# Performance work log

Measured on AMD Instinct MI355X. Metric: run time of the kernel, lower is better.

The kernel has to match this reference:

```python
import jax, jax.numpy as jnp
import numpy as np

P = 16        # patch size
B = 32        # batch
HW = 224      # image height/width
EMB = 768     # embedding dim
CN = (512, 2048, 8192)  # cluster counts
D = 3 * P * P  # patch feature dim = 768


def setup_inputs() -> dict:
    key = jax.random.key(0)
    ks = jax.random.split(key, 7)
    return {
        "data": jax.random.normal(ks[0], (B, 3, HW, HW), jnp.float32),
        "c0": jax.random.normal(ks[1], (CN[0], D), jnp.float32),
        "c1": jax.random.normal(ks[2], (CN[1], D), jnp.float32),
        "c2": jax.random.normal(ks[3], (CN[2], D), jnp.float32),
        "e0": jax.random.normal(ks[4], (CN[0], EMB), jnp.float32),
        "e1": jax.random.normal(ks[5], (CN[1], EMB), jnp.float32),
        "e2": jax.random.normal(ks[6], (CN[2], EMB), jnp.float32),
    }


def _classify(x, center):
    scores = -2.0 * (x @ center.T) + jnp.sum(center * center, axis=-1)  # [b, n, K]
    cls = jnp.argmin(scores, axis=-1)                                   # [b, n]
    img = center[cls]                                                   # nearest-center gather
    return cls, x - img, img


def reference(data, c0, c1, c2, e0, e1, e2):
    b, c, h, w = data.shape
    hp = h // P
    wp = w // P
    # b c (h hp) (w wp) -> b (h w) (c hp wp)
    x = data.reshape(b, c, hp, P, wp, P).transpose(0, 2, 4, 1, 3, 5).reshape(b, hp * wp, c * P * P)

    cls0, diff, img0 = _classify(x, c0)
    cls1, diff, img1 = _classify(diff, c1)
    cls2, diff, img2 = _classify(diff, c2)

    # reconstruct image from summed center patches: b (h w) (c hp wp) -> b c (h hp) (w wp)
    img_sum = (img0 + img1 + img2).reshape(b, hp, wp, c, P, P).transpose(0, 3, 1, 4, 2, 5).reshape(b, c, h, w)
    # residual: b (h w) c -> b c h w
    diff_out = diff.reshape(b, hp, wp, -1).transpose(0, 3, 1, 2)

    # embedding lookups (the only grad-carrying path in the torch module)
    embed = e0[cls0] + e1[cls1] + e2[cls2]          # [b, hp*wp, EMB]
    embed = embed.reshape(b, hp, wp, -1).transpose(0, 3, 1, 2)  # [b, EMB, hp, wp]

    # quantization branch is under torch.no_grad()
    return (embed, jax.lax.stop_gradient(img_sum), jax.lax.stop_gradient(diff_out))
```

## Files before the change

kernel.cpp:

```cpp
#include <hip/hip_runtime.h>
#include <stdint.h>

#define BATCH 32
#define HWD 224
#define HP 14
#define NP (BATCH * HP * HP)
#define DIM 768
#define K0 512
#define K1 2048
#define K2 8192
#define KTOT (K0 + K1 + K2)

typedef unsigned long long ull;
typedef unsigned int uint;
typedef __attribute__((ext_vector_type(8))) short bf16x8;
typedef __attribute__((ext_vector_type(4))) float f32x4;

__device__ __forceinline__ uint fkey(float f) {
    uint u = __float_as_uint(f);
    return (u & 0x80000000u) ? ~u : (u | 0x80000000u);
}
__device__ __forceinline__ short f2bf(float f) {
    uint u = __float_as_uint(f);
    uint r = (u + 0x7fffu + ((u >> 16) & 1u)) >> 16;
    return (short)r;
}
__device__ __forceinline__ float bf2f(short h) {
    return __uint_as_float(((uint)(unsigned short)h) << 16);
}
__device__ __forceinline__ ull umin64(ull a, ull b) { return a < b ? a : b; }
__device__ __forceinline__ ull umax64(ull a, ull b) { return a > b ? a : b; }

__global__ void patchify_split_kernel(const float* __restrict__ data,
                                      short* __restrict__ xh, short* __restrict__ xl) {
    int gid = blockIdx.x * 256 + threadIdx.x;
    int d = gid % DIM;
    int p = gid / DIM;
    int b = p / 196; int t = p % 196; int i = t / 14, j = t % 14;
    int ch = d >> 8; int r = d & 255; int py = r >> 4; int px = r & 15;
    float v = data[((b * 3 + ch) * HWD + i * 16 + py) * HWD + j * 16 + px];
    short h = f2bf(v);
    xh[gid] = h;
    xl[gid] = f2bf(v - bf2f(h));
}

__global__ void cprep_all_kernel(const float* __restrict__ c0, const float* __restrict__ c1,
                                 const float* __restrict__ c2,
                                 short* __restrict__ ch, float* __restrict__ nrm) {
    int lane = threadIdx.x & 63;
    int row = blockIdx.x * 4 + (threadIdx.x >> 6);
    const float* src;
    if (row < K0)           src = c0 + (size_t)row * DIM;
    else if (row < K0 + K1) src = c1 + (size_t)(row - K0) * DIM;
    else                    src = c2 + (size_t)(row - K0 - K1) * DIM;
    float s = 0.f;
    #pragma unroll
    for (int i = 0; i < 12; ++i) {
        int d = lane + i * 64;
        float v = src[d];
        ch[(size_t)row * DIM + d] = f2bf(v);
        s += v * v;
    }
    #pragma unroll
    for (int off = 32; off; off >>= 1) s += __shfl_xor(s, off, 64);
    if (lane == 0) nrm[row] = s;
}

__global__ __launch_bounds__(256, 2) void classify16(
    const short* __restrict__ xh,
    const short* __restrict__ chv,
    const float* __restrict__ nrm,
    ull* __restrict__ partB, ull* __restrict__ partS2)
{
    constexpr int NHT = 8;
    constexpr int NB = 256;
    constexpr int CH0 = 512;
    constexpr int SLOTS = 512 + 128 * NHT;
    constexpr int NJ = 6;
    constexpr int GX = NP / 128;
    __shared__ __align__(16) short lds[3 * SLOTS * 8];

    int bx = blockIdx.x, by = blockIdx.y;
    if ((gridDim.y & 7) == 0) {
        int P = blockIdx.x + GX * blockIdx.y;
        int xcd = P & 7;
        int wofs = P >> 3;
        int ypx = gridDim.y >> 3;
        by = xcd * ypx + (wofs % ypx);
        bx = wofs / ypx;
    }

    const int tid = threadIdx.x;
    const int lane = tid & 63;
    const int w = tid >> 6;
    const int wm = w & 1, wn = w >> 1;
    const int pbase = bx * 128;
    const int n0 = by * NB;

    const short* gp[NJ];
    int ls[NJ];
    #pragma unroll
    for (int j = 0; j < NJ; ++j) {
        int g = j * 4 + w;
        const short* base; int rb, sb, t;
        if (g < 8) { base = xh;  rb = pbase; sb = 0;    t = g; }
        else       { base = chv; rb = n0;    sb = CH0;  t = g - 8; }
        gp[j] = base + (size_t)(rb + t * 16 + (lane & 15)) * DIM + ((lane >> 4) * 8);
        ls[j] = sb + t * 64;
    }

    f32x4 acc[4][NHT];
    #pragma unroll
    for (int i = 0; i < 4; ++i)
        #pragma unroll
        for (int u = 0; u < NHT; ++u) acc[i][u] = (f32x4){0.f, 0.f, 0.f, 0.f};

    auto stage = [&](int buf, int kt) {
        const int off = buf * SLOTS;
        #pragma unroll
        for (int j = 0; j < NJ; ++j) {
            __builtin_amdgcn_global_load_lds(
                (const __attribute__((address_space(1))) void*)(gp[j] + kt * 32),
                (__attribute__((address_space(3))) void*)(lds + (size_t)(off + ls[j]) * 8),
                16, 0, 0);
        }
    };
    auto compute = [&](int buf) {
        const bf16x8* Lc = (const bf16x8*)lds + buf * SLOTS;
        bf16x8 fxh[4];
        #pragma unroll
        for (int i = 0; i < 4; ++i)
            fxh[i] = Lc[(wm * 4 + i) * 64 + lane];
        #pragma unroll
        for (int u = 0; u < NHT; ++u) {
            bf16x8 fch = Lc[CH0 + (wn * NHT + u) * 64 + lane];
            #pragma unroll
            for (int i = 0; i < 4; ++i)
                acc[i][u] = __builtin_amdgcn_mfma_f32_16x16x32_bf16(fxh[i], fch, acc[i][u], 0, 0, 0);
        }
    };

    stage(0, 0);
    stage(1, 1);
    asm volatile("s_waitcnt vmcnt(6)" ::: "memory");
    __builtin_amdgcn_s_barrier();
    __builtin_amdgcn_sched_barrier(0);

    #pragma unroll 3
    for (int t = 0; t < 24; ++t) {
        if (t + 2 < 24) stage((t + 2) % 3, t + 2);
        compute(t % 3);
        if (t < 23) {
            if (t + 2 < 24) asm volatile("s_waitcnt vmcnt(6)" ::: "memory");
            else            asm volatile("s_waitcnt vmcnt(0)" ::: "memory");
            __builtin_amdgcn_s_barrier();
            __builtin_amdgcn_sched_barrier(0);
        }
    }

    float nor[NHT]; uint ncol[NHT];
    #pragma unroll
    for (int u = 0; u < NHT; ++u) {
        ncol[u] = (uint)(n0 + (wn * NHT + u) * 16 + (lane & 15));
        nor[u] = nrm[ncol[u]];
    }
    const int pw = 2 * gridDim.y;
    #pragma unroll
    for (int i = 0; i < 4; ++i) {
        #pragma unroll
        for (int reg = 0; reg < 4; ++reg) {
            ull b = ~0ull, s2 = ~0ull;
            #pragma unroll
            for (int u = 0; u < NHT; ++u) {
                float s = fmaf(-2.f, acc[i][u][reg], nor[u]);
                ull pk = ((ull)fkey(s) << 32) | ncol[u];
                ull nb = umin64(b, pk);
                s2 = umin64(s2, umax64(b, pk));
                b = nb;
            }
            #pragma unroll
            for (int off = 1; off <= 8; off <<= 1) {
                ull ob = __shfl_xor(b, off, 64);
                ull os2 = __shfl_xor(s2, off, 64);
                ull nb = umin64(b, ob);
                s2 = umin64(umin64(s2, os2), umax64(b, ob));
                b = nb;
            }
            if ((lane & 15) == 0) {
                int row = pbase + (wm * 4 + i) * 16 + (lane >> 4) * 4 + reg;
                size_t o = (size_t)row * pw + (size_t)by * 2 + wn;
                partB[o] = b;
                partS2[o] = s2;
            }
        }
    }
}

__global__ void merge_rescue_update(
    short* __restrict__ xh, short* __restrict__ xl,
    const float* __restrict__ cent, const float* __restrict__ nrm,
    const ull* __restrict__ partB, const ull* __restrict__ partS2,
    int nsplit, int* __restrict__ cls)
{
    int lane = threadIdx.x & 63;
    int p = blockIdx.x * 4 + (threadIdx.x >> 6);
    ull a = ~0ull, c = ~0ull;
    for (int j = lane; j < nsplit; j += 64) {
        ull b2 = partB[(size_t)p * nsplit + j];
        ull s2b = partS2[(size_t)p * nsplit + j];
        ull na = umin64(a, b2);
        c = umin64(umin64(c, s2b), umax64(a, b2));
        a = na;
    }
    int idx[4];
    #pragma unroll
    for (int r = 0; r < 4; ++r) {
        ull m = a;
        #pragma unroll
        for (int off = 32; off; off >>= 1) m = umin64(m, __shfl_xor(m, off, 64));
        idx[r] = (int)(m & 0xFFFFFFFFull);
        if (a == m) { a = c; c = ~0ull; }
    }
    float xv[12];
    #pragma unroll
    for (int i = 0; i < 12; ++i) {
        int d = lane + i * 64;
        xv[i] = bf2f(xh[(size_t)p * DIM + d]) + bf2f(xl[(size_t)p * DIM + d]);
    }
    float dot[4] = {0.f, 0.f, 0.f, 0.f};
    #pragma unroll
    for (int r = 0; r < 4; ++r) {
        const float* cr = cent + (size_t)idx[r] * DIM;
        #pragma unroll
        for (int i = 0; i < 12; ++i) dot[r] = fmaf(xv[i], cr[lane + i * 64], dot[r]);
    }
    #pragma unroll
    for (int r = 0; r < 4; ++r)
        #pragma unroll
        for (int off = 32; off; off >>= 1) dot[r] += __shfl_xor(dot[r], off, 64);
    ull best = ~0ull;
    #pragma unroll
    for (int r = 0; r < 4; ++r) {
        float sc = fmaf(-2.f, dot[r], nrm[idx[r]]);
        best = umin64(best, ((ull)fkey(sc) << 32) | (uint)idx[r]);
    }
    int cw = (int)(best & 0xFFFFFFFFull);
    if (lane == 0) cls[p] = cw;
    const float* cwr = cent + (size_t)cw * DIM;
    #pragma unroll
    for (int i = 0; i < 12; ++i) {
        int d = lane + i * 64;
        float nx = xv[i] - cwr[d];
        short h = f2bf(nx);
        xh[(size_t)p * DIM + d] = h;
        xl[(size_t)p * DIM + d] = f2bf(nx - bf2f(h));
    }
}

__global__ void embdiff_kernel(const short* __restrict__ xh, const short* __restrict__ xl,
    const int* __restrict__ cls0, const int* __restrict__ cls1, const int* __restrict__ cls2,
    const float* __restrict__ e0, const float* __restrict__ e1, const float* __restrict__ e2,
    float* __restrict__ out)
{
    __shared__ float s[196][65];
    int b = blockIdx.x / 12;
    int dc = (blockIdx.x % 12) * 64;
    int tid = threadIdx.x;
    int dl = tid & 63;
    for (int it = 0; it < 49; ++it) {
        int pl = it * 4 + (tid >> 6);
        int p = b * 196 + pl;
        int d = dc + dl;
        s[pl][dl] = e0[(size_t)cls0[p] * DIM + d] + e1[(size_t)cls1[p] * DIM + d]
                  + e2[(size_t)cls2[p] * DIM + d];
    }
    __syncthreads();
    if (tid < 196) {
        for (int d = 0; d < 64; ++d)
            out[((size_t)b * DIM + dc + d) * 196 + tid] = s[tid][d];
    }
    __syncthreads();
    for (int it = 0; it < 49; ++it) {
        int pl = it * 4 + (tid >> 6);
        size_t o = (size_t)(b * 196 + pl) * DIM + dc + dl;
        s[pl][dl] = bf2f(xh[o]) + bf2f(xl[o]);
    }
    __syncthreads();
    if (tid < 196) {
        float* od = out + 2 * (size_t)NP * DIM;
        for (int d = 0; d < 64; ++d)
            od[((size_t)b * DIM + dc + d) * 196 + tid] = s[tid][d];
    }
}

__global__ void img_kernel(
    const int* __restrict__ cls0, const int* __restrict__ cls1, const int* __restrict__ cls2,
    const float* __restrict__ c0, const float* __restrict__ c1, const float* __restrict__ c2,
    float* __restrict__ out)
{
    __shared__ float s[14][256];
    int bi = blockIdx.x;
    int b = bi / 42; int rem = bi % 42; int ch = rem / 14; int i = rem % 14;
    int tid = threadIdx.x;
    for (int j = 0; j < 14; ++j) {
        int p = b * 196 + i * 14 + j;
        int d = ch * 256 + tid;
        s[j][tid] = c0[(size_t)cls0[p] * DIM + d] + c1[(size_t)cls1[p] * DIM + d]
                  + c2[(size_t)cls2[p] * DIM + d];
    }
    __syncthreads();
    float* oi = out + (size_t)NP * DIM;
    if (tid < 224) {
        int j = tid >> 4, px = tid & 15;
        for (int py = 0; py < 16; ++py)
            oi[(((size_t)b * 3 + ch) * HWD + i * 16 + py) * HWD + tid] = s[j][py * 16 + px];
    }
}

extern "C" void kernel_launch(void* const* d_in, const int* in_sizes, int n_in,
                              void* d_out, int out_size, void* d_ws, size_t ws_size,
                              hipStream_t stream) {
    const float* data = (const float*)d_in[0];
    const float* c0 = (const float*)d_in[1];
    const float* c1 = (const float*)d_in[2];
    const float* c2 = (const float*)d_in[3];
    const float* e0 = (const float*)d_in[4];
    const float* e1 = (const float*)d_in[5];
    const float* e2 = (const float*)d_in[6];
    float* out = (float*)d_out;

    char* w = (char*)d_ws;
    short* xh = (short*)w;    w += (size_t)NP * DIM * 2;
    short* xl = (short*)w;    w += (size_t)NP * DIM * 2;
    short* chB = (short*)w;   w += (size_t)KTOT * DIM * 2;
    float* nrm = (float*)w;   w += (size_t)KTOT * 4;
    ull* partB = (ull*)w;     w += (size_t)NP * 128 * 8;
    ull* partS2 = (ull*)w;    w += (size_t)NP * 128 * 8;
    int* cls0 = (int*)w;      w += (size_t)NP * 4;
    int* cls1 = (int*)w;      w += (size_t)NP * 4;
    int* cls2 = (int*)w;      w += (size_t)NP * 4;

    patchify_split_kernel<<<(NP * DIM) / 256, 256, 0, stream>>>(data, xh, xl);
    cprep_all_kernel<<<KTOT / 4, 256, 0, stream>>>(c0, c1, c2, chB, nrm);

    classify16<<<dim3(NP / 128, K0 / 256), 256, 0, stream>>>(
        xh, chB, nrm, partB, partS2);
    merge_rescue_update<<<NP / 4, 256, 0, stream>>>(xh, xl, c0, nrm, partB, partS2, 4, cls0);

    classify16<<<dim3(NP / 128, K1 / 256), 256, 0, stream>>>(
        xh, chB + (size_t)K0 * DIM, nrm + K0, partB, partS2);
    merge_rescue_update<<<NP / 4, 256, 0, stream>>>(xh, xl, c1, nrm + K0, partB, partS2, 16, cls1);

    classify16<<<dim3(NP / 128, K2 / 256), 256, 0, stream>>>(
        xh, chB + (size_t)(K0 + K1) * DIM, nrm + K0 + K1, partB, partS2);
    merge_rescue_update<<<NP / 4, 256, 0, stream>>>(xh, xl, c2, nrm + K0 + K1, partB, partS2, 64, cls2);

    embdiff_kernel<<<BATCH * 12, 256, 0, stream>>>(xh, xl, cls0, cls1, cls2, e0, e1, e2, out);
    img_kernel<<<BATCH * 3 * 14, 256, 0, stream>>>(cls0, cls1, cls2, c0, c1, c2, out);
}
```

Baseline: 433.6 us.

## Switch classify GEMM to double-buffered LDS with 3 blocks per SM

Cuts the LDS staging ring from three buffers to two and raises launch bounds from 2 to 3 blocks per CU, so more waves can hide latency. Global load base pointers are made wave-uniform through readfirstlane and a shared per-lane offset, to save VGPRs. The loop now issues one stage ahead with plain __syncthreads instead of fine-grained vmcnt waits. Each wave has less prefetch depth, and every barrier now waits for the whole load to finish, which can expose memory latency.

```diff
diff --git a/kernel.cpp b/kernel.cpp
--- a/kernel.cpp
+++ b/kernel.cpp
@@ -66,7 +66,7 @@
     if (lane == 0) nrm[row] = s;
 }
 
-__global__ __launch_bounds__(256, 2) void classify16(
+__global__ __launch_bounds__(256, 3) void classify16(
     const short* __restrict__ xh,
     const short* __restrict__ chv,
     const float* __restrict__ nrm,
@@ -78,7 +78,7 @@
     constexpr int SLOTS = 512 + 128 * NHT;
     constexpr int NJ = 6;
     constexpr int GX = NP / 128;
-    __shared__ __align__(16) short lds[3 * SLOTS * 8];
+    __shared__ __align__(16) short lds[2 * SLOTS * 8];
 
     int bx = blockIdx.x, by = blockIdx.y;
     if ((gridDim.y & 7) == 0) {
@@ -97,16 +97,20 @@
     const int pbase = bx * 128;
     const int n0 = by * NB;
 
-    const short* gp[NJ];
-    int ls[NJ];
+    const short* gbase[NJ];
+    int lsl[NJ];
+    const int laneoff = (lane & 15) * DIM + ((lane >> 4) * 8);
     #pragma unroll
     for (int j = 0; j < NJ; ++j) {
         int g = j * 4 + w;
         const short* base; int rb, sb, t;
         if (g < 8) { base = xh;  rb = pbase; sb = 0;    t = g; }
         else       { base = chv; rb = n0;    sb = CH0;  t = g - 8; }
-        gp[j] = base + (size_t)(rb + t * 16 + (lane & 15)) * DIM + ((lane >> 4) * 8);
-        ls[j] = sb + t * 64;
+        ull b64 = (ull)(base + (size_t)(rb + t * 16) * DIM);
+        uint lo = __builtin_amdgcn_readfirstlane((uint)b64);
+        uint hi = __builtin_amdgcn_readfirstlane((uint)(b64 >> 32));
+        gbase[j] = (const short*)(((ull)hi << 32) | lo);
+        lsl[j] = __builtin_amdgcn_readfirstlane(sb + t * 64);
     }
 
     f32x4 acc[4][NHT];
@@ -120,8 +124,8 @@
         #pragma unroll
         for (int j = 0; j < NJ; ++j) {
             __builtin_amdgcn_global_load_lds(
-                (const __attribute__((address_space(1))) void*)(gp[j] + kt * 32),
-                (__attribute__((address_space(3))) void*)(lds + (size_t)(off + ls[j]) * 8),
+                (const __attribute__((address_space(1))) void*)(gbase[j] + laneoff + kt * 32),
+                (__attribute__((address_space(3))) void*)(lds + (size_t)(off + lsl[j]) * 8),
                 16, 0, 0);
         }
     };
@@ -141,21 +145,12 @@
     };
 
     stage(0, 0);
-    stage(1, 1);
-    asm volatile("s_waitcnt vmcnt(6)" ::: "memory");
-    __builtin_amdgcn_s_barrier();
-    __builtin_amdgcn_sched_barrier(0);
-
-    #pragma unroll 3
+    __syncthreads();
+    #pragma unroll 4
     for (int t = 0; t < 24; ++t) {
-        if (t + 2 < 24) stage((t + 2) % 3, t + 2);
-        compute(t % 3);
-        if (t < 23) {
-            if (t + 2 < 24) asm volatile("s_waitcnt vmcnt(6)" ::: "memory");
-            else            asm volatile("s_waitcnt vmcnt(0)" ::: "memory");
-            __builtin_amdgcn_s_barrier();
-            __builtin_amdgcn_sched_barrier(0);
-        }
+        if (t + 1 < 24) stage((t + 1) & 1, t + 1);
+        compute(t & 1);
+        if (t < 23) __syncthreads();
     }
 
     float nor[NHT]; uint ncol[NHT];
```

Measured after the change: 758.8 us. 1.75x slower.
